# Kernel tuning notes

Hardware: AMD Instinct MI355X
Metric: run time of the kernel (lower is better)

## Reference

```python
import jax, jax.numpy as jnp
import numpy as np

THRESHOLD_IOU = 0.8  # forward default in the original module


def setup_inputs() -> dict:
    key = jax.random.key(0)
    k1, k2, k3, k4 = jax.random.split(key, 4)
    N = M = 16
    H = W = 768
    # Binary masks (the original zeroes pixels to 0.0 and tests >0 via torch.where)
    masks_a = (jax.random.uniform(k1, (N, H, W)) > 0.6).astype(jnp.float32)
    masks_b = (jax.random.uniform(k2, (M, H, W)) > 0.6).astype(jnp.float32)
    # Make a few masks identical across labels so the IoU>threshold (suppression)
    # branch is exercised, not just the partial-overlap zeroing branch.
    masks_b = masks_b.at[:4].set(masks_a[:4])
    scores_a = jax.random.uniform(k3, (N,))
    scores_b = jax.random.uniform(k4, (M,))
    return {"masks_a": masks_a, "masks_b": masks_b,
            "scores_a": scores_a, "scores_b": scores_b}


def _overlap_filter(masks_a, masks_b, scores_a, scores_b, thr):
    # Sequential pairwise IoU + overlap zeroing, faithful to the original
    # nested product(enumerate(masks), enumerate(other_masks)) loop order
    # (i outer, j inner), where each pair sees masks already modified by
    # earlier pairs. Pruning ("keep") is applied after the loop; here it is
    # represented with static shapes as keep flags + zeroed-out rows.
    N, H, W = masks_a.shape
    M = masks_b.shape[0]
    P = H * W
    A0 = masks_a.reshape(N, P)
    B0 = masks_b.reshape(M, P)

    def body(carry, k):
        A, B, fi, fj = carry
        i = k // M
        j = k % M
        a = A[i]  # [P]
        b = B[j]  # [P]
        abin = a > 0
        bbin = b > 0
        inter = abin & bbin
        inter_sum = jnp.sum(inter.astype(jnp.float32))
        union_sum = jnp.sum((abin | bbin).astype(jnp.float32))
        iou = inter_sum / jnp.maximum(union_sum, 1.0)
        a_wins = scores_a[i] > scores_b[j]
        suppress = iou > thr                 # mark whole loser mask for removal
        zero_case = (iou > 0) & ~suppress    # zero overlapped pixels of loser
        b_new = jnp.where(zero_case & a_wins & inter, 0.0, b)
        a_new = jnp.where(zero_case & (~a_wins) & inter, 0.0, a)
        A = A.at[i].set(a_new)
        B = B.at[j].set(b_new)
        fj = fj.at[j].set(fj[j] | (suppress & a_wins))
        fi = fi.at[i].set(fi[i] | (suppress & ~a_wins))
        return (A, B, fi, fj), None

    fi0 = jnp.zeros(N, dtype=bool)
    fj0 = jnp.zeros(M, dtype=bool)
    (A, B, fi, fj), _ = jax.lax.scan(body, (A0, B0, fi0, fj0), jnp.arange(N * M))
    keep_a = ~fi
    keep_b = ~fj
    A = jnp.where(keep_a[:, None], A, 0.0)
    B = jnp.where(keep_b[:, None], B, 0.0)
    return A.reshape(N, H, W), B.reshape(M, H, W), keep_a, keep_b


def reference(masks_a, masks_b, scores_a, scores_b):
    return _overlap_filter(masks_a, masks_b, scores_a, scores_b, THRESHOLD_IOU)
```

## Files before the change

kernel.cpp:

```cpp
#include <hip/hip_runtime.h>
#include <stdint.h>

#define NM 16
#define HW_P 589824
#define U8PM 9216
#define C4PM 4608
#define F4PM 147456
#define F4PT 2359296
#define PT 512
#define NG 8
#define EWG 64

typedef unsigned long long u64;
typedef float vf4 __attribute__((ext_vector_type(4)));


__device__ __forceinline__ unsigned aload(const unsigned* p) {
    return __hip_atomic_load(p, __ATOMIC_RELAXED, __HIP_MEMORY_SCOPE_AGENT);
}
__device__ __forceinline__ void astore(unsigned* p, unsigned v) {
    __hip_atomic_store(p, v, __ATOMIC_RELAXED, __HIP_MEMORY_SCOPE_AGENT);
}
__device__ __forceinline__ unsigned afadd(unsigned* p, unsigned v) {
    return __hip_atomic_fetch_add(p, v, __ATOMIC_RELAXED, __HIP_MEMORY_SCOPE_AGENT);
}

__device__ __forceinline__ uint32_t spread4(uint32_t x) {
    uint32_t t = (x | (x << 12)) & 0x000F000Fu;
    t = (t | (t << 6)) & 0x03030303u;
    t = (t | (t << 3)) & 0x11111111u;
    return t;
}

__global__ __launch_bounds__(256) void binarize_kernel(
    const float* __restrict__ ma, const float* __restrict__ mb,
    uint32_t* __restrict__ bitsA, uint32_t* __restrict__ bitsB,
    uint4* __restrict__ meta4)
{
    if (blockIdx.x == 0) {
        uint4 z; z.x = z.y = z.z = z.w = 0u;
        meta4[threadIdx.x] = z;
        meta4[threadIdx.x + 256] = z;
    }
    int g = blockIdx.x * 256 + threadIdx.x;
    int tensor = (g >= F4PT);
    int lg = tensor ? (g - F4PT) : g;
    const float* src = tensor ? mb : ma;
    vf4 v = __builtin_nontemporal_load(((const vf4*)src) + lg);
    u64 q0 = __ballot(v.x > 0.0f);
    u64 q1 = __ballot(v.y > 0.0f);
    u64 q2 = __ballot(v.z > 0.0f);
    u64 q3 = __ballot(v.w > 0.0f);
    int lane = threadIdx.x & 63;
    if (lane < 8) {
        uint32_t wd = spread4((uint32_t)(q0 >> (8 * lane)) & 0xFFu)
                    | (spread4((uint32_t)(q1 >> (8 * lane)) & 0xFFu) << 1)
                    | (spread4((uint32_t)(q2 >> (8 * lane)) & 0xFFu) << 2)
                    | (spread4((uint32_t)(q3 >> (8 * lane)) & 0xFFu) << 3);
        uint32_t* bits = tensor ? bitsB : bitsA;
        bits[((lg & ~63) >> 3) + lane] = wd;
    }
}

__global__ __launch_bounds__(PT, 1) void pipeline_kernel(
    const float* __restrict__ sa, const float* __restrict__ sb,
    uint32_t* bitsA, uint32_t* bitsB, unsigned* meta, u64* msg)
{
    unsigned* cnt    = meta;
    unsigned* winner = meta + 8;
    int* flagsA      = (int*)(meta + 16);
    int* flagsB      = (int*)(meta + 32);
    unsigned* prodF  = meta + 80;

    const int tid = threadIdx.x;
    const int wave = tid >> 6, lane = tid & 63;

    __shared__ int s_g;
    __shared__ int4 part[8];

    if (tid == 0) {
        int xcc;
        asm volatile("s_getreg_b32 %0, hwreg(HW_REG_XCC_ID)" : "=s"(xcc));
        xcc &= 7;
        unsigned slot = afadd(&cnt[xcc], 1u);
        int mine = -1;
        if (slot < NG) {
            if (slot == NG - 1) {
                unsigned exp = 0u;
                __hip_atomic_compare_exchange_strong(
                    winner, &exp, (unsigned)(xcc + 1),
                    __ATOMIC_RELAXED, __ATOMIC_RELAXED, __HIP_MEMORY_SCOPE_AGENT);
            }
            unsigned w;
            while (!(w = aload(winner))) __builtin_amdgcn_s_sleep(1);
            if (w == (unsigned)(xcc + 1)) mine = (int)slot;
        }
        s_g = mine;
    }
    __syncthreads();
    const int g = s_g;
    if (g < 0) return;

    const int c0 = 2 * g, c1 = 2 * g + 1;
    uint4* A4 = (uint4*)bitsA;
    uint4* B4 = (uint4*)bitsB;

    u64 b0[18], b1[18];

    int v0 = 0, v1 = 0;
#pragma unroll
    for (int w = 0; w < 9; ++w) {
        uint4 q0 = B4[(size_t)c0 * C4PM + tid + PT * w];
        uint4 q1 = B4[(size_t)c1 * C4PM + tid + PT * w];
        b0[2 * w] = ((u64)q0.y << 32) | q0.x; b0[2 * w + 1] = ((u64)q0.w << 32) | q0.z;
        b1[2 * w] = ((u64)q1.y << 32) | q1.x; b1[2 * w + 1] = ((u64)q1.w << 32) | q1.z;
        v0 += __popcll(b0[2 * w]) + __popcll(b0[2 * w + 1]);
        v1 += __popcll(b1[2 * w]) + __popcll(b1[2 * w + 1]);
    }
#pragma unroll
    for (int off = 32; off >= 1; off >>= 1) {
        v0 += __shfl_xor(v0, off); v1 += __shfl_xor(v1, off);
    }
    if (lane == 0) { int4 p; p.x = v0; p.y = v1; p.z = 0; p.w = 0; part[wave] = p; }
    __syncthreads();
    int pcb0 = 0, pcb1 = 0;
#pragma unroll
    for (int w = 0; w < 8; ++w) { pcb0 += part[w].x; pcb1 += part[w].y; }
    float sb0 = sb[c0], sb1 = sb[c1];
    int fb0 = 0, fb1 = 0;
    __syncthreads();

    for (int t = 0; t < NM; ++t) {
        int pca, fa;
        u64 a[18];

        if (g == 0) {
            pca = 0; fa = 0;
#pragma unroll
            for (int w = 0; w < 9; ++w) {
                uint4 q = A4[(size_t)t * C4PM + tid + PT * w];
                a[2 * w] = ((u64)q.y << 32) | q.x;
                a[2 * w + 1] = ((u64)q.w << 32) | q.z;
            }
        } else {
            const unsigned* fptr = &prodF[((g - 1) * 16 + t) * 4];
            unsigned v;
            do { v = aload(fptr); } while (!v);
            asm volatile("" ::: "memory");
            pca = (int)((v >> 1) & 0xFFFFFu);
            fa  = (int)((v >> 21) & 1u);
            const uint4* s4 = (const uint4*)(msg + (size_t)((g - 1) * 16 + t) * U8PM);
#pragma unroll
            for (int w = 0; w < 9; ++w) {
                uint4 q = s4[tid + PT * w];
                a[2 * w]     = ((u64)q.y << 32) | q.x;
                a[2 * w + 1] = ((u64)q.w << 32) | q.z;
            }
        }

        int i0 = 0, i1 = 0, itr = 0, ipc = 0;
#pragma unroll
        for (int w = 0; w < 18; ++w) {
            u64 ab0 = a[w] & b0[w];
            i0 += __popcll(ab0);
            i1 += __popcll(a[w] & b1[w]);
            itr += __popcll(ab0 & b1[w]);
        }
        if (g == 0) {
#pragma unroll
            for (int w = 0; w < 18; ++w) ipc += __popcll(a[w]);
        }
#pragma unroll
        for (int off = 32; off >= 1; off >>= 1) {
            i0 += __shfl_xor(i0, off); i1 += __shfl_xor(i1, off);
            itr += __shfl_xor(itr, off); ipc += __shfl_xor(ipc, off);
        }
        if (lane == 0) {
            int4 p; p.x = i0; p.y = i1; p.z = itr; p.w = ipc; part[wave] = p;
        }
        __syncthreads();
        int I0 = 0, I1 = 0, T = 0, PC = 0;
#pragma unroll
        for (int w = 0; w < 8; ++w) {
            int4 p = part[w];
            I0 += p.x; I1 += p.y; T += p.z; PC += p.w;
        }
        if (g == 0) pca = PC;

        float sai = sa[t];
        bool aupd = false;
        {
            int inter = I0;
            int uni = pca + pcb0 - inter;
            float iou = (float)inter / fmaxf((float)uni, 1.0f);
            bool aw = sai > sb0;
            if (iou > 0.8f) { if (aw) fb0 = 1; else fa = 1; }
            else if (inter > 0) {
                if (aw) {
                    pcb0 -= inter;
#pragma unroll
                    for (int w = 0; w < 18; ++w) b0[w] &= ~a[w];
                } else {
                    pca -= inter; aupd = true;
#pragma unroll
                    for (int w = 0; w < 18; ++w) a[w] &= ~b0[w];
                }
            }
        }
        {
            int inter = aupd ? (I1 - T) : I1;
            int uni = pca + pcb1 - inter;
            float iou = (float)inter / fmaxf((float)uni, 1.0f);
            bool aw = sai > sb1;
            if (iou > 0.8f) { if (aw) fb1 = 1; else fa = 1; }
            else if (inter > 0) {
                if (aw) {
                    pcb1 -= inter;
#pragma unroll
                    for (int w = 0; w < 18; ++w) b1[w] &= ~a[w];
                } else {
                    pca -= inter;
#pragma unroll
                    for (int w = 0; w < 18; ++w) a[w] &= ~b1[w];
                }
            }
        }

        if (g < NG - 1) {
            uint4* so = (uint4*)(msg + (size_t)(g * 16 + t) * U8PM);
#pragma unroll
            for (int w = 0; w < 9; ++w) {
                uint4 q;
                q.x = (uint32_t)a[2 * w];     q.y = (uint32_t)(a[2 * w] >> 32);
                q.z = (uint32_t)a[2 * w + 1]; q.w = (uint32_t)(a[2 * w + 1] >> 32);
                so[tid + PT * w] = q;
            }
            __syncthreads();
            if (tid == 0)
                astore(&prodF[(g * 16 + t) * 4],
                       1u | ((unsigned)pca << 1) | ((unsigned)fa << 21));
        } else {
            uint4* Ar = A4 + (size_t)t * C4PM;
#pragma unroll
            for (int w = 0; w < 9; ++w) {
                uint4 q;
                q.x = (uint32_t)a[2 * w];     q.y = (uint32_t)(a[2 * w] >> 32);
                q.z = (uint32_t)a[2 * w + 1]; q.w = (uint32_t)(a[2 * w + 1] >> 32);
                Ar[tid + PT * w] = q;
            }
            if (tid == 0) flagsA[t] = fa;
            __syncthreads();
        }
    }

    uint4* Wc0 = B4 + (size_t)c0 * C4PM;
    uint4* Wc1 = B4 + (size_t)c1 * C4PM;
#pragma unroll
    for (int w = 0; w < 9; ++w) {
        uint4 q0, q1;
        q0.x = (uint32_t)b0[2 * w];     q0.y = (uint32_t)(b0[2 * w] >> 32);
        q0.z = (uint32_t)b0[2 * w + 1]; q0.w = (uint32_t)(b0[2 * w + 1] >> 32);
        q1.x = (uint32_t)b1[2 * w];     q1.y = (uint32_t)(b1[2 * w] >> 32);
        q1.z = (uint32_t)b1[2 * w + 1]; q1.w = (uint32_t)(b1[2 * w + 1] >> 32);
        Wc0[tid + PT * w] = q0;
        Wc1[tid + PT * w] = q1;
    }
    if (tid == 0) { flagsB[c0] = fb0; flagsB[c1] = fb1; }
}

__global__ __launch_bounds__(256) void expand_kernel(
    const uint32_t* __restrict__ bitsA, const uint32_t* __restrict__ bitsB,
    const int* __restrict__ meta, float* __restrict__ out)
{
    int g = blockIdx.x * 256 + threadIdx.x;
    int tensor = (g >= F4PT);
    int lg = tensor ? (g - F4PT) : g;
    const uint32_t* bits = tensor ? bitsB : bitsA;
    const int* flags = meta + (tensor ? 32 : 16);
    int m = lg / F4PM;
    bool keep = (flags[m] == 0);
    uint32_t wd = keep ? bits[lg >> 3] : 0u;
    int sh = (lg & 7) * 4;
    vf4 o;
    o.x = ((wd >> (sh + 0)) & 1u) ? 1.0f : 0.0f;
    o.y = ((wd >> (sh + 1)) & 1u) ? 1.0f : 0.0f;
    o.z = ((wd >> (sh + 2)) & 1u) ? 1.0f : 0.0f;
    o.w = ((wd >> (sh + 3)) & 1u) ? 1.0f : 0.0f;
    __builtin_nontemporal_store(o, ((vf4*)out) + g);
    if (g < 2 * NM) {
        out[(size_t)2 * NM * HW_P + g] = meta[16 + g] ? 0.0f : 1.0f;
    }
}

extern "C" void kernel_launch(void* const* d_in, const int* in_sizes, int n_in,
                              void* d_out, int out_size, void* d_ws, size_t ws_size,
                              hipStream_t stream)
{
    const float* ma = (const float*)d_in[0];
    const float* mb = (const float*)d_in[1];
    const float* sa = (const float*)d_in[2];
    const float* sb = (const float*)d_in[3];
    float* out = (float*)d_out;
    char* ws = (char*)d_ws;

    uint32_t* bitsA = (uint32_t*)(ws);
    uint32_t* bitsB = (uint32_t*)(ws + 1179648);
    unsigned* meta  = (unsigned*)(ws + 2359296);
    u64* msg        = (u64*)(ws + 2367488);

    binarize_kernel<<<18432, 256, 0, stream>>>(ma, mb, bitsA, bitsB,
                                               (uint4*)meta);
    pipeline_kernel<<<EWG, PT, 0, stream>>>(sa, sb, bitsA, bitsB, meta, msg);
    expand_kernel<<<18432, 256, 0, stream>>>(bitsA, bitsB, (const int*)meta, out);
}
```

Measured before the change: 219.6 us.

## Use per-wave flags and double-buffered messages in the inter-block pipeline

Replaces the block-wide producer flag with one flag per wave, so each consumer wave waits only for the matching producer wave instead of a whole-block barrier. The message buffer shrinks from one slot per step to two ring slots per stage, guarded by per-wave ack counters, which keeps the working set small and cache-resident. Loads use the sc0 cache modifier and the trailing __syncthreads is dropped; the LDS partials array is double-buffered so the per-iteration barrier can be skipped. The risk is subtle ordering bugs around the ring reuse and flag visibility, plus added spin traffic.

Measured after the change: 227.5 us. 3.6% more time.

```diff
diff --git a/kernel.cpp b/kernel.cpp
--- a/kernel.cpp
+++ b/kernel.cpp
@@ -25,6 +25,9 @@
     return __hip_atomic_fetch_add(p, v, __ATOMIC_RELAXED, __HIP_MEMORY_SCOPE_AGENT);
 }
 
+#define LOAD16_SC0(dst, addr) \
+    asm volatile("global_load_dwordx4 %0, %1, off sc0" : "=v"(dst) : "v"(addr))
+
 __device__ __forceinline__ uint32_t spread4(uint32_t x) {
     uint32_t t = (x | (x << 12)) & 0x000F000Fu;
     t = (t | (t << 6)) & 0x03030303u;
@@ -41,6 +44,8 @@
         uint4 z; z.x = z.y = z.z = z.w = 0u;
         meta4[threadIdx.x] = z;
         meta4[threadIdx.x + 256] = z;
+        meta4[threadIdx.x + 512] = z;
+        meta4[threadIdx.x + 768] = z;
     }
     int g = blockIdx.x * 256 + threadIdx.x;
     int tensor = (g >= F4PT);
@@ -70,13 +75,14 @@
     unsigned* winner = meta + 8;
     int* flagsA      = (int*)(meta + 16);
     int* flagsB      = (int*)(meta + 32);
-    unsigned* prodF  = meta + 80;
+    unsigned* ackF   = meta + 64;
+    unsigned* prodF  = meta + 512;
 
     const int tid = threadIdx.x;
     const int wave = tid >> 6, lane = tid & 63;
 
     __shared__ int s_g;
-    __shared__ int4 part[8];
+    __shared__ int4 part[2][8];
 
     if (tid == 0) {
         int xcc;
@@ -104,6 +110,8 @@
     const int c0 = 2 * g, c1 = 2 * g + 1;
     uint4* A4 = (uint4*)bitsA;
     uint4* B4 = (uint4*)bitsB;
+    unsigned* ackO = ackF + (g * 8 + wave) * 4;
+    unsigned* ackI = ackF + ((g - 1) * 8 + wave) * 4;
 
     u64 b0[18], b1[18];
 
@@ -121,41 +129,44 @@
     for (int off = 32; off >= 1; off >>= 1) {
         v0 += __shfl_xor(v0, off); v1 += __shfl_xor(v1, off);
     }
-    if (lane == 0) { int4 p; p.x = v0; p.y = v1; p.z = 0; p.w = 0; part[wave] = p; }
+    if (lane == 0) { int4 p; p.x = v0; p.y = v1; p.z = 0; p.w = 0; part[0][wave] = p; }
     __syncthreads();
     int pcb0 = 0, pcb1 = 0;
 #pragma unroll
-    for (int w = 0; w < 8; ++w) { pcb0 += part[w].x; pcb1 += part[w].y; }
+    for (int w = 0; w < 8; ++w) { pcb0 += part[0][w].x; pcb1 += part[0][w].y; }
     float sb0 = sb[c0], sb1 = sb[c1];
     int fb0 = 0, fb1 = 0;
     __syncthreads();
 
     for (int t = 0; t < NM; ++t) {
         int pca, fa;
-        u64 a[18];
+        uint4 q[9];
 
         if (g == 0) {
             pca = 0; fa = 0;
 #pragma unroll
-            for (int w = 0; w < 9; ++w) {
-                uint4 q = A4[(size_t)t * C4PM + tid + PT * w];
-                a[2 * w] = ((u64)q.y << 32) | q.x;
-                a[2 * w + 1] = ((u64)q.w << 32) | q.z;
-            }
+            for (int w = 0; w < 9; ++w)
+                q[w] = A4[(size_t)t * C4PM + tid + PT * w];
         } else {
-            const unsigned* fptr = &prodF[((g - 1) * 16 + t) * 4];
+            const unsigned* fptr = &prodF[(((g - 1) * 16 + t) * 8 + wave) * 4];
             unsigned v;
             do { v = aload(fptr); } while (!v);
             asm volatile("" ::: "memory");
             pca = (int)((v >> 1) & 0xFFFFFu);
             fa  = (int)((v >> 21) & 1u);
-            const uint4* s4 = (const uint4*)(msg + (size_t)((g - 1) * 16 + t) * U8PM);
-#pragma unroll
-            for (int w = 0; w < 9; ++w) {
-                uint4 q = s4[tid + PT * w];
-                a[2 * w]     = ((u64)q.y << 32) | q.x;
-                a[2 * w + 1] = ((u64)q.w << 32) | q.z;
-            }
+            const uint4* s4 = (const uint4*)(msg + (size_t)((g - 1) * 2 + (t & 1)) * U8PM);
+#pragma unroll
+            for (int w = 0; w < 9; ++w)
+                LOAD16_SC0(q[w], s4 + tid + PT * w);
+            asm volatile("s_waitcnt vmcnt(0)" ::: "memory");
+            __builtin_amdgcn_sched_barrier(0);
+            if (lane == 0) astore(ackI, (unsigned)(t + 1));
+        }
+        u64 a[18];
+#pragma unroll
+        for (int w = 0; w < 9; ++w) {
+            a[2 * w]     = ((u64)q[w].y << 32) | q[w].x;
+            a[2 * w + 1] = ((u64)q[w].w << 32) | q[w].z;
         }
 
         int i0 = 0, i1 = 0, itr = 0, ipc = 0;
@@ -176,13 +187,14 @@
             itr += __shfl_xor(itr, off); ipc += __shfl_xor(ipc, off);
         }
         if (lane == 0) {
-            int4 p; p.x = i0; p.y = i1; p.z = itr; p.w = ipc; part[wave] = p;
+            int4 p; p.x = i0; p.y = i1; p.z = itr; p.w = ipc;
+            part[t & 1][wave] = p;
         }
         __syncthreads();
         int I0 = 0, I1 = 0, T = 0, PC = 0;
 #pragma unroll
         for (int w = 0; w < 8; ++w) {
-            int4 p = part[w];
+            int4 p = part[t & 1][w];
             I0 += p.x; I1 += p.y; T += p.z; PC += p.w;
         }
         if (g == 0) pca = PC;
@@ -227,29 +239,32 @@
         }
 
         if (g < NG - 1) {
-            uint4* so = (uint4*)(msg + (size_t)(g * 16 + t) * U8PM);
+            if (t >= 2) {
+                while ((int)aload(ackO) < t - 1) {}
+            }
+            asm volatile("" ::: "memory");
+            uint4* so = (uint4*)(msg + (size_t)(g * 2 + (t & 1)) * U8PM);
 #pragma unroll
             for (int w = 0; w < 9; ++w) {
-                uint4 q;
-                q.x = (uint32_t)a[2 * w];     q.y = (uint32_t)(a[2 * w] >> 32);
-                q.z = (uint32_t)a[2 * w + 1]; q.w = (uint32_t)(a[2 * w + 1] >> 32);
-                so[tid + PT * w] = q;
-            }
-            __syncthreads();
-            if (tid == 0)
-                astore(&prodF[(g * 16 + t) * 4],
+                uint4 o;
+                o.x = (uint32_t)a[2 * w];     o.y = (uint32_t)(a[2 * w] >> 32);
+                o.z = (uint32_t)a[2 * w + 1]; o.w = (uint32_t)(a[2 * w + 1] >> 32);
+                so[tid + PT * w] = o;
+            }
+            asm volatile("s_waitcnt vmcnt(0)" ::: "memory");
+            if (lane == 0)
+                astore(&prodF[((g * 16 + t) * 8 + wave) * 4],
                        1u | ((unsigned)pca << 1) | ((unsigned)fa << 21));
         } else {
             uint4* Ar = A4 + (size_t)t * C4PM;
 #pragma unroll
             for (int w = 0; w < 9; ++w) {
-                uint4 q;
-                q.x = (uint32_t)a[2 * w];     q.y = (uint32_t)(a[2 * w] >> 32);
-                q.z = (uint32_t)a[2 * w + 1]; q.w = (uint32_t)(a[2 * w + 1] >> 32);
-                Ar[tid + PT * w] = q;
+                uint4 o;
+                o.x = (uint32_t)a[2 * w];     o.y = (uint32_t)(a[2 * w] >> 32);
+                o.z = (uint32_t)a[2 * w + 1]; o.w = (uint32_t)(a[2 * w + 1] >> 32);
+                Ar[tid + PT * w] = o;
             }
             if (tid == 0) flagsA[t] = fa;
-            __syncthreads();
         }
     }
 
@@ -306,7 +321,7 @@
     uint32_t* bitsA = (uint32_t*)(ws);
     uint32_t* bitsB = (uint32_t*)(ws + 1179648);
     unsigned* meta  = (unsigned*)(ws + 2359296);
-    u64* msg        = (u64*)(ws + 2367488);
+    u64* msg        = (u64*)(ws + 2375680);
 
     binarize_kernel<<<18432, 256, 0, stream>>>(ma, mb, bitsA, bitsB,
                                                (uint4*)meta);
```
